# Performance work log

Hardware: AMD Instinct MI355X
Metric: run time of the kernel (lower is better)

## Reference

```python
import jax, jax.numpy as jnp
import numpy as np


def setup_inputs() -> dict:
    key = jax.random.key(0)
    ks = jax.random.split(key, 6)
    B, T, S, E, D = 8, 128, 512, 512, 512  # batch, trg_len, src_len, enc_dim, trg_dim
    W_SCALE = 0.03  # small init to keep tanh unsaturated
    return {
        "hidden": jax.random.normal(ks[0], (B, T, D), jnp.float32),
        "encoder_outputs": jax.random.normal(ks[1], (B, S, E), jnp.float32),
        "encoder_mask": jnp.ones((B, S), jnp.float32),
        "W_attn": jax.random.normal(ks[2], (D, E + D), jnp.float32) * W_SCALE,
        "b_attn": jnp.zeros((D,), jnp.float32),
        "W_v": jax.random.normal(ks[3], (1, D), jnp.float32) * W_SCALE,
        "b_v": jnp.zeros((1,), jnp.float32),
        "W_out": jax.random.normal(ks[4], (D, E + D), jnp.float32) * W_SCALE,
    }


def masked_softmax(x, m, axis=-1):
    # faithful to repo: x*m, stable exp, e*m, normalize with eps
    x = x * m
    e_x = jnp.exp(x - jnp.max(x, axis=axis, keepdims=True))
    e_x = e_x * m
    return e_x / (jnp.sum(e_x, axis=axis, keepdims=True) + 1e-6)


def reference(hidden, encoder_outputs, encoder_mask, W_attn, b_attn, W_v, b_v, W_out):
    B, T, D = hidden.shape
    S = encoder_outputs.shape[1]
    # concat order in get_energy is (hidden_i, encoder_outputs), so split W_attn
    W_h = W_attn[:, :D]   # (D_out, trg_dim)
    W_e = W_attn[:, D:]   # (D_out, enc_dim)
    # Linear(concat) == h@W_h^T + e@W_e^T + b; vectorized over all (t, s) pairs
    hp = jnp.einsum('btd,kd->btk', hidden, W_h)            # (B,T,K)
    ep = jnp.einsum('bse,ke->bsk', encoder_outputs, W_e)   # (B,S,K)
    feat = jnp.tanh(hp[:, :, None, :] + ep[:, None, :, :] + b_attn)  # (B,T,S,K)
    energies = jnp.einsum('btsk,k->bts', feat, W_v[0]) + b_v[0]      # (B,T,S)
    # forward: energies * mask, then masked softmax
    m = encoder_mask[:, None, :]  # (B,1,S)
    energies = energies * m
    attn_weights = masked_softmax(energies, m, axis=-1)    # (B,T,S)
    weighted_context = jnp.einsum('bts,bse->bte', attn_weights, encoder_outputs)
    h_cat = jnp.concatenate([weighted_context, hidden], axis=-1)  # (B,T,E+D)
    h_tilde = jnp.tanh(jnp.einsum('btc,dc->btd', h_cat, W_out))   # (B,T,D)
    return h_tilde, weighted_context, attn_weights
```

## Files before the change

### kernel.cpp

```cpp
#include <hip/hip_runtime.h>
#include <hip/hip_bf16.h>
#include <math.h>

typedef unsigned short u16;
typedef unsigned int u32;
typedef __bf16 bf16x8 __attribute__((ext_vector_type(8)));
typedef float f32x4 __attribute__((ext_vector_type(4)));

#define OUT_WC   524288LL
#define OUT_ATTN 1048576LL
#define C2 2.8853900817779268f
#define LOG2E 1.4426950408889634f
#define LAS 40

#define P_ENC    0LL
#define P_HID    2097152LL
#define P_WATTN  2621440LL
#define P_WOUTR  3145728LL
#define P_WOUTTL 3407872LL

__device__ inline u16 f2b(float f) {
    return (u16)((__float_as_uint(f) + 0x8000u) >> 16);
}
__device__ inline float b2f(u16 v) { return __uint_as_float(((u32)v) << 16); }
__device__ inline u32 pkcvt(float x, float y) {
    __hip_bfloat162 h = __float22bfloat162_rn(make_float2(x, y));
    return *(u32*)&h;
}
__device__ inline float tanh_fast(float x) {
    return 1.f - 2.f * __builtin_amdgcn_rcpf(__builtin_amdgcn_exp2f(C2 * x) + 1.f);
}

__global__ __launch_bounds__(256) void tobf(
    const float* __restrict__ enc, const float* __restrict__ hidden,
    const float* __restrict__ Wattn, const float* __restrict__ Wout,
    u16* __restrict__ dst)
{
    const int tid = threadIdx.x;
    if (blockIdx.x < 1664) {
        long long i = ((long long)blockIdx.x * 256 + tid) * 8;
        const float* src;
        if (i < 2097152)      src = enc + i;
        else if (i < 2621440) src = hidden + (i - 2097152);
        else if (i < 3145728) src = Wattn + (i - 2621440);
        else {
            long long j = i - 3145728;
            src = Wout + ((j >> 9) << 10) + 512 + (j & 511);
        }
        float4 v0 = *(const float4*)src;
        float4 v1 = *(const float4*)(src + 4);
        *(uint4*)(dst + i) = make_uint4(pkcvt(v0.x, v0.y), pkcvt(v0.z, v0.w),
                                        pkcvt(v1.x, v1.y), pkcvt(v1.z, v1.w));
    } else {
        __shared__ u32 lt[64 * 66];
        int tt = blockIdx.x - 1664;
        int n0 = (tt >> 3) * 64, d0 = (tt & 7) * 64;
        int r = tid >> 2, c = (tid & 3) * 16;
        const float* sp = Wout + (long long)(n0 + r) * 1024 + d0 + c;
        #pragma unroll
        for (int q = 0; q < 4; ++q) {
            float4 v = *(const float4*)(sp + q * 4);
            lt[r * 66 + c + q * 4 + 0] = f2b(v.x);
            lt[r * 66 + c + q * 4 + 1] = f2b(v.y);
            lt[r * 66 + c + q * 4 + 2] = f2b(v.z);
            lt[r * 66 + c + q * 4 + 3] = f2b(v.w);
        }
        __syncthreads();
        int dr = tid >> 2, nc = (tid & 3) * 16;
        u32 o[8];
        #pragma unroll
        for (int q = 0; q < 8; ++q) {
            u32 lo = lt[(nc + 2 * q) * 66 + dr];
            u32 hi = lt[(nc + 2 * q + 1) * 66 + dr];
            o[q] = lo | (hi << 16);
        }
        u16* dp = dst + P_WOUTTL + (long long)(d0 + dr) * 512 + n0 + nc;
        *(uint4*)dp       = make_uint4(o[0], o[1], o[2], o[3]);
        *(uint4*)(dp + 8) = make_uint4(o[4], o[5], o[6], o[7]);
    }
}

__global__ __launch_bounds__(256) void proj(
    const u16* __restrict__ pool, const float* __restrict__ battn,
    float* __restrict__ hp, u16* __restrict__ ept, float* __restrict__ hh)
{
    __shared__ u16 lA[64 * LAS];
    __shared__ u16 lB[64 * LAS];
    const int tid = threadIdx.x;
    const int wvi = tid >> 6, ln = tid & 63;
    const int wm = wvi >> 1, wn = wvi & 1;
    const int l16 = ln & 15, quad = ln >> 4;
    const int blk = blockIdx.x;
    int bx, by, zz = 0, lda, ldb, mode;
    const u16 *A, *B;
    if (blk < 512) {
        mode = 0;
        zz = blk >> 6; by = (blk >> 3) & 7; bx = blk & 7;
        A = pool + P_WATTN + 512; lda = 1024;
        B = pool + P_ENC + (long long)zz * 262144; ldb = 512;
    } else if (blk < 640) {
        mode = 1;
        int i = blk - 512; by = i >> 3; bx = i & 7;
        A = pool + P_HID; lda = 512;
        B = pool + P_WATTN; ldb = 1024;
    } else {
        mode = 2;
        int i = blk - 640; by = i >> 3; bx = i & 7;
        A = pool + P_HID; lda = 512;
        B = pool + P_WOUTR; ldb = 512;
    }
    const int m0 = by * 64, n0 = bx * 64;
    const int srow = tid >> 2, skof = (tid & 3) * 8;
    const u16* Ap = A + (long long)(m0 + srow) * lda + skof;
    const u16* Bp = B + (long long)(n0 + srow) * ldb + skof;

    f32x4 acc00 = {0,0,0,0}, acc01 = {0,0,0,0}, acc10 = {0,0,0,0}, acc11 = {0,0,0,0};

    for (int k0 = 0; k0 < 512; k0 += 32) {
        uint4 av = *(const uint4*)(Ap + k0);
        uint4 bv = *(const uint4*)(Bp + k0);
        __syncthreads();
        *(uint4*)&lA[srow * LAS + skof] = av;
        *(uint4*)&lB[srow * LAS + skof] = bv;
        __syncthreads();
        bf16x8 a0 = *(const bf16x8*)&lA[(wm * 32      + l16) * LAS + quad * 8];
        bf16x8 a1 = *(const bf16x8*)&lA[(wm * 32 + 16 + l16) * LAS + quad * 8];
        bf16x8 b0 = *(const bf16x8*)&lB[(wn * 32      + l16) * LAS + quad * 8];
        bf16x8 b1 = *(const bf16x8*)&lB[(wn * 32 + 16 + l16) * LAS + quad * 8];
        acc00 = __builtin_amdgcn_mfma_f32_16x16x32_bf16(a0, b0, acc00, 0, 0, 0);
        acc01 = __builtin_amdgcn_mfma_f32_16x16x32_bf16(a0, b1, acc01, 0, 0, 0);
        acc10 = __builtin_amdgcn_mfma_f32_16x16x32_bf16(a1, b0, acc10, 0, 0, 0);
        acc11 = __builtin_amdgcn_mfma_f32_16x16x32_bf16(a1, b1, acc11, 0, 0, 0);
    }

    const f32x4* accs[4] = { &acc00, &acc01, &acc10, &acc11 };
    #pragma unroll
    for (int i = 0; i < 2; ++i) {
        #pragma unroll
        for (int j = 0; j < 2; ++j) {
            const f32x4& a = *accs[i * 2 + j];
            #pragma unroll
            for (int r = 0; r < 4; ++r) {
                int m = m0 + wm * 32 + i * 16 + quad * 4 + r;
                int n = n0 + wn * 32 + j * 16 + l16;
                float v = a[r];
                if (mode == 0)
                    ept[(long long)zz * 262144 + (long long)m * 512 + n] =
                        f2b(__builtin_amdgcn_exp2f(C2 * v));
                else if (mode == 1)
                    hp[(long long)m * 512 + n] = C2 * (v + battn[n]);
                else
                    hh[(long long)m * 512 + n] = v;
            }
        }
    }
}

__device__ inline float wred_sum(float v) {
    #pragma unroll
    for (int i = 32; i > 0; i >>= 1) v += __shfl_xor(v, i);
    return v;
}
__device__ inline float bred_sum8(float v, float* red, int tid) {
    v = wred_sum(v);
    __syncthreads();
    if ((tid & 63) == 0) red[tid >> 6] = v;
    __syncthreads();
    float s = 0.f;
    #pragma unroll
    for (int i = 0; i < 8; ++i) s += red[i];
    return s;
}
__device__ inline void bred2_max(float v0, float v1, float* red, int tid,
                                 float* o0, float* o1) {
    #pragma unroll
    for (int i = 32; i > 0; i >>= 1) {
        v0 = fmaxf(v0, __shfl_xor(v0, i));
        v1 = fmaxf(v1, __shfl_xor(v1, i));
    }
    __syncthreads();
    if ((tid & 63) == 0) { red[tid >> 6] = v0; red[8 + (tid >> 6)] = v1; }
    __syncthreads();
    float a0 = red[0], a1 = red[8];
    #pragma unroll
    for (int i = 1; i < 8; ++i) { a0 = fmaxf(a0, red[i]); a1 = fmaxf(a1, red[8 + i]); }
    *o0 = a0; *o1 = a1;
}
__device__ inline void bred2_sum(float v0, float v1, float* red, int tid,
                                 float* o0, float* o1) {
    #pragma unroll
    for (int i = 32; i > 0; i >>= 1) { v0 += __shfl_xor(v0, i); v1 += __shfl_xor(v1, i); }
    __syncthreads();
    if ((tid & 63) == 0) { red[tid >> 6] = v0; red[8 + (tid >> 6)] = v1; }
    __syncthreads();
    float a0 = 0.f, a1 = 0.f;
    #pragma unroll
    for (int i = 0; i < 8; ++i) { a0 += red[i]; a1 += red[8 + i]; }
    *o0 = a0; *o1 = a1;
}

__device__ inline void proc8(uint4 c, float4 hw, float* a0, float* a1) {
    u32 cc[4] = {c.x, c.y, c.z, c.w};
    #pragma unroll
    for (int i = 0; i < 4; ++i) {
        float xl = __uint_as_float(cc[i] << 16);
        float xh = __uint_as_float(cc[i] & 0xFFFF0000u);
        float rl0 = __builtin_amdgcn_rcpf(fmaf(hw.x, xl, 1.f));
        float rh0 = __builtin_amdgcn_rcpf(fmaf(hw.x, xh, 1.f));
        float rl1 = __builtin_amdgcn_rcpf(fmaf(hw.y, xl, 1.f));
        float rh1 = __builtin_amdgcn_rcpf(fmaf(hw.y, xh, 1.f));
        a0[2*i]   = fmaf(hw.z, rl0, a0[2*i]);
        a0[2*i+1] = fmaf(hw.z, rh0, a0[2*i+1]);
        a1[2*i]   = fmaf(hw.z, rl1, a1[2*i]);
        a1[2*i+1] = fmaf(hw.z, rh1, a1[2*i+1]);
    }
}

__global__ __launch_bounds__(512) void energies(
    const float* __restrict__ maskp, const float* __restrict__ hp,
    const u16* __restrict__ ept, const float* __restrict__ Wv,
    const float* __restrict__ bvp, const u16* __restrict__ pool,
    float* __restrict__ out)
{
    __shared__ __align__(16) float4 hpw[512];
    __shared__ float pa[2][8][512];
    __shared__ __align__(16) float2 aL[512];
    __shared__ __align__(16) float2 wcL[512];
    __shared__ float red[16];
    const int tid = threadIdx.x;
    const int b = blockIdx.x >> 6;
    const int t0 = (blockIdx.x & 63) * 2;
    const u16* enc_bf = pool + P_ENC;
    const u16* woutT  = pool + P_WOUTTL;

    float w = Wv[tid];
    float h0 = hp[(long long)(b * 128 + t0) * 512 + tid];
    float h1 = hp[(long long)(b * 128 + t0 + 1) * 512 + tid];
    hpw[tid] = make_float4(__builtin_amdgcn_exp2f(h0), __builtin_amdgcn_exp2f(h1), w, 0.f);
    float sumWv = bred_sum8(w, red, tid);

    const int kg = tid >> 6, sl = tid & 63;
    const int s0 = sl * 8;
    const u16* eb = ept + (long long)b * 262144 + (kg * 64) * 512 + s0;
    const float4* hq = &hpw[kg * 64];

    float a0[8] = {0,0,0,0,0,0,0,0}, a1[8] = {0,0,0,0,0,0,0,0};
    uint4 c0 = *(const uint4*)(eb);
    uint4 c1 = *(const uint4*)(eb + 512);
    uint4 c2 = *(const uint4*)(eb + 1024);
    uint4 c3 = *(const uint4*)(eb + 1536);
    for (int kk = 0; kk < 60; kk += 4) {
        const u16* nb = eb + (kk + 4) * 512;
        uint4 n0 = *(const uint4*)(nb);
        uint4 n1 = *(const uint4*)(nb + 512);
        uint4 n2 = *(const uint4*)(nb + 1024);
        uint4 n3 = *(const uint4*)(nb + 1536);
        proc8(c0, hq[kk],     a0, a1);
        proc8(c1, hq[kk + 1], a0, a1);
        proc8(c2, hq[kk + 2], a0, a1);
        proc8(c3, hq[kk + 3], a0, a1);
        c0 = n0; c1 = n1; c2 = n2; c3 = n3;
    }
    proc8(c0, hq[60], a0, a1);
    proc8(c1, hq[61], a0, a1);
    proc8(c2, hq[62], a0, a1);
    proc8(c3, hq[63], a0, a1);

    *(float4*)&pa[0][kg][s0]     = make_float4(a0[0], a0[1], a0[2], a0[3]);
    *(float4*)&pa[0][kg][s0 + 4] = make_float4(a0[4], a0[5], a0[6], a0[7]);
    *(float4*)&pa[1][kg][s0]     = make_float4(a1[0], a1[1], a1[2], a1[3]);
    *(float4*)&pa[1][kg][s0 + 4] = make_float4(a1[4], a1[5], a1[6], a1[7]);
    __syncthreads();

    const int s = tid;
    float A0 = 0.f, A1 = 0.f;
    #pragma unroll
    for (int g = 0; g < 8; ++g) { A0 += pa[0][g][s]; A1 += pa[1][g][s]; }
    float mv = maskp[(long long)b * 512 + s];
    float bv0 = bvp[0];
    float r0 = (bv0 + sumWv - 2.f * A0) * mv; r0 *= mv;
    float r1 = (bv0 + sumWv - 2.f * A1) * mv; r1 *= mv;

    float mx0, mx1;
    bred2_max(r0, r1, red, tid, &mx0, &mx1);
    float ex0 = __builtin_amdgcn_exp2f((r0 - mx0) * LOG2E) * mv;
    float ex1 = __builtin_amdgcn_exp2f((r1 - mx1) * LOG2E) * mv;
    float sm0, sm1;
    bred2_sum(ex0, ex1, red, tid, &sm0, &sm1);
    float at0 = ex0 * (1.f / (sm0 + 1e-6f));
    float at1 = ex1 * (1.f / (sm1 + 1e-6f));
    out[OUT_ATTN + (long long)(b * 128 + t0) * 512 + s]     = at0;
    out[OUT_ATTN + (long long)(b * 128 + t0 + 1) * 512 + s] = at1;
    aL[s] = make_float2(at0, at1);
    __syncthreads();

    {
        const u16* encb = enc_bf + (long long)b * 262144 + tid;
        const float4* aL4 = (const float4*)aL;
        float acc0 = 0.f, acc1 = 0.f;
        for (int ss = 0; ss < 512; ss += 8) {
            float ev[8];
            #pragma unroll
            for (int i = 0; i < 8; ++i) ev[i] = b2f(encb[(ss + i) * 512]);
            #pragma unroll
            for (int i = 0; i < 4; ++i) {
                float4 ap = aL4[(ss >> 1) + i];
                acc0 = fmaf(ap.x, ev[2*i],   acc0);
                acc1 = fmaf(ap.y, ev[2*i],   acc1);
                acc0 = fmaf(ap.z, ev[2*i+1], acc0);
                acc1 = fmaf(ap.w, ev[2*i+1], acc1);
            }
        }
        out[OUT_WC + (long long)(b * 128 + t0) * 512 + tid]     = acc0;
        out[OUT_WC + (long long)(b * 128 + t0 + 1) * 512 + tid] = acc1;
        wcL[tid] = make_float2(acc0, acc1);
    }
    __syncthreads();

    {
        const u16* wt = woutT + tid;
        const float4* wL4 = (const float4*)wcL;
        float acc0 = 0.f, acc1 = 0.f;
        for (int dd = 0; dd < 512; dd += 8) {
            float wv[8];
            #pragma unroll
            for (int i = 0; i < 8; ++i) wv[i] = b2f(wt[(dd + i) * 512]);
            #pragma unroll
            for (int i = 0; i < 4; ++i) {
                float4 cp = wL4[(dd >> 1) + i];
                acc0 = fmaf(cp.x, wv[2*i],   acc0);
                acc1 = fmaf(cp.y, wv[2*i],   acc1);
                acc0 = fmaf(cp.z, wv[2*i+1], acc0);
                acc1 = fmaf(cp.w, wv[2*i+1], acc1);
            }
        }
        long long o0 = (long long)(b * 128 + t0) * 512 + tid;
        long long o1 = (long long)(b * 128 + t0 + 1) * 512 + tid;
        out[o0] = tanh_fast(acc0 + out[o0]);
        out[o1] = tanh_fast(acc1 + out[o1]);
    }
}

extern "C" void kernel_launch(void* const* d_in, const int* in_sizes, int n_in,
                              void* d_out, int out_size, void* d_ws, size_t ws_size,
                              hipStream_t stream)
{
    const float* hidden = (const float*)d_in[0];
    const float* enc    = (const float*)d_in[1];
    const float* mask   = (const float*)d_in[2];
    const float* Wattn  = (const float*)d_in[3];
    const float* battn  = (const float*)d_in[4];
    const float* Wv     = (const float*)d_in[5];
    const float* bvp    = (const float*)d_in[6];
    const float* Wout   = (const float*)d_in[7];
    float* out = (float*)d_out;

    float* hp  = (float*)d_ws;
    u16*   ept = (u16*)((char*)d_ws + (2 << 20));
    u16*   pool = (u16*)((char*)d_ws + (6 << 20));

    tobf<<<1728, 256, 0, stream>>>(enc, hidden, Wattn, Wout, pool);
    proj<<<768, 256, 0, stream>>>(pool, battn, hp, ept, out );
    energies<<<512, 512, 0, stream>>>(mask, hp, ept, Wv, bvp, pool, out);
}
```

Before: 153.5 us.

## Double energies block threads with split-K reductions and prefetch proj GEMM tiles

```diff
diff --git a/kernel.cpp b/kernel.cpp
--- a/kernel.cpp
+++ b/kernel.cpp
@@ -11,7 +11,7 @@
 #define OUT_ATTN 1048576LL
 #define C2 2.8853900817779268f
 #define LOG2E 1.4426950408889634f
-#define LAS 40
+#define PLAS 72
 
 #define P_ENC    0LL
 #define P_HID    2097152LL
@@ -84,8 +84,8 @@
     const u16* __restrict__ pool, const float* __restrict__ battn,
     float* __restrict__ hp, u16* __restrict__ ept, float* __restrict__ hh)
 {
-    __shared__ u16 lA[64 * LAS];
-    __shared__ u16 lB[64 * LAS];
+    __shared__ u16 lA[64 * PLAS];
+    __shared__ u16 lB[64 * PLAS];
     const int tid = threadIdx.x;
     const int wvi = tid >> 6, ln = tid & 63;
     const int wm = wvi >> 1, wn = wvi & 1;
@@ -110,40 +110,51 @@
         B = pool + P_WOUTR; ldb = 512;
     }
     const int m0 = by * 64, n0 = bx * 64;
-    const int srow = tid >> 2, skof = (tid & 3) * 8;
-    const u16* Ap = A + (long long)(m0 + srow) * lda + skof;
-    const u16* Bp = B + (long long)(n0 + srow) * ldb + skof;
-
-    f32x4 acc00 = {0,0,0,0}, acc01 = {0,0,0,0}, acc10 = {0,0,0,0}, acc11 = {0,0,0,0};
-
-    for (int k0 = 0; k0 < 512; k0 += 32) {
-        uint4 av = *(const uint4*)(Ap + k0);
-        uint4 bv = *(const uint4*)(Bp + k0);
-        __syncthreads();
-        *(uint4*)&lA[srow * LAS + skof] = av;
-        *(uint4*)&lB[srow * LAS + skof] = bv;
-        __syncthreads();
-        bf16x8 a0 = *(const bf16x8*)&lA[(wm * 32      + l16) * LAS + quad * 8];
-        bf16x8 a1 = *(const bf16x8*)&lA[(wm * 32 + 16 + l16) * LAS + quad * 8];
-        bf16x8 b0 = *(const bf16x8*)&lB[(wn * 32      + l16) * LAS + quad * 8];
-        bf16x8 b1 = *(const bf16x8*)&lB[(wn * 32 + 16 + l16) * LAS + quad * 8];
-        acc00 = __builtin_amdgcn_mfma_f32_16x16x32_bf16(a0, b0, acc00, 0, 0, 0);
-        acc01 = __builtin_amdgcn_mfma_f32_16x16x32_bf16(a0, b1, acc01, 0, 0, 0);
-        acc10 = __builtin_amdgcn_mfma_f32_16x16x32_bf16(a1, b0, acc10, 0, 0, 0);
-        acc11 = __builtin_amdgcn_mfma_f32_16x16x32_bf16(a1, b1, acc11, 0, 0, 0);
-    }
-
-    const f32x4* accs[4] = { &acc00, &acc01, &acc10, &acc11 };
+    const int sr = tid >> 2, sc = (tid & 3) * 16;
+    const u16* Ap = A + (long long)(m0 + sr) * lda + sc;
+    const u16* Bp = B + (long long)(n0 + sr) * ldb + sc;
+
+    f32x4 acc[2][2] = {};
+    uint4 ra0 = *(const uint4*)(Ap);
+    uint4 ra1 = *(const uint4*)(Ap + 8);
+    uint4 rb0 = *(const uint4*)(Bp);
+    uint4 rb1 = *(const uint4*)(Bp + 8);
+
+    for (int k0 = 0; k0 < 512; k0 += 64) {
+        __syncthreads();
+        *(uint4*)&lA[sr * PLAS + sc]     = ra0;
+        *(uint4*)&lA[sr * PLAS + sc + 8] = ra1;
+        *(uint4*)&lB[sr * PLAS + sc]     = rb0;
+        *(uint4*)&lB[sr * PLAS + sc + 8] = rb1;
+        __syncthreads();
+        if (k0 < 448) {
+            ra0 = *(const uint4*)(Ap + k0 + 64);
+            ra1 = *(const uint4*)(Ap + k0 + 72);
+            rb0 = *(const uint4*)(Bp + k0 + 64);
+            rb1 = *(const uint4*)(Bp + k0 + 72);
+        }
+        #pragma unroll
+        for (int kk = 0; kk < 2; ++kk) {
+            bf16x8 a0 = *(const bf16x8*)&lA[(wm * 32      + l16) * PLAS + kk * 32 + quad * 8];
+            bf16x8 a1 = *(const bf16x8*)&lA[(wm * 32 + 16 + l16) * PLAS + kk * 32 + quad * 8];
+            bf16x8 b0 = *(const bf16x8*)&lB[(wn * 32      + l16) * PLAS + kk * 32 + quad * 8];
+            bf16x8 b1 = *(const bf16x8*)&lB[(wn * 32 + 16 + l16) * PLAS + kk * 32 + quad * 8];
+            acc[0][0] = __builtin_amdgcn_mfma_f32_16x16x32_bf16(a0, b0, acc[0][0], 0, 0, 0);
+            acc[0][1] = __builtin_amdgcn_mfma_f32_16x16x32_bf16(a0, b1, acc[0][1], 0, 0, 0);
+            acc[1][0] = __builtin_amdgcn_mfma_f32_16x16x32_bf16(a1, b0, acc[1][0], 0, 0, 0);
+            acc[1][1] = __builtin_amdgcn_mfma_f32_16x16x32_bf16(a1, b1, acc[1][1], 0, 0, 0);
+        }
+    }
+
     #pragma unroll
     for (int i = 0; i < 2; ++i) {
         #pragma unroll
         for (int j = 0; j < 2; ++j) {
-            const f32x4& a = *accs[i * 2 + j];
             #pragma unroll
             for (int r = 0; r < 4; ++r) {
                 int m = m0 + wm * 32 + i * 16 + quad * 4 + r;
                 int n = n0 + wn * 32 + j * 16 + l16;
-                float v = a[r];
+                float v = acc[i][j][r];
                 if (mode == 0)
                     ept[(long long)zz * 262144 + (long long)m * 512 + n] =
                         f2b(__builtin_amdgcn_exp2f(C2 * v));
@@ -161,42 +172,42 @@
     for (int i = 32; i > 0; i >>= 1) v += __shfl_xor(v, i);
     return v;
 }
-__device__ inline float bred_sum8(float v, float* red, int tid) {
+__device__ inline float wred_max(float v) {
+    #pragma unroll
+    for (int i = 32; i > 0; i >>= 1) v = fmaxf(v, __shfl_xor(v, i));
+    return v;
+}
+__device__ inline float bred_sum16(float v, float* red, int tid) {
     v = wred_sum(v);
     __syncthreads();
     if ((tid & 63) == 0) red[tid >> 6] = v;
     __syncthreads();
     float s = 0.f;
     #pragma unroll
-    for (int i = 0; i < 8; ++i) s += red[i];
+    for (int i = 0; i < 16; ++i) s += red[i];
     return s;
 }
-__device__ inline void bred2_max(float v0, float v1, float* red, int tid,
-                                 float* o0, float* o1) {
-    #pragma unroll
-    for (int i = 32; i > 0; i >>= 1) {
-        v0 = fmaxf(v0, __shfl_xor(v0, i));
-        v1 = fmaxf(v1, __shfl_xor(v1, i));
-    }
-    __syncthreads();
-    if ((tid & 63) == 0) { red[tid >> 6] = v0; red[8 + (tid >> 6)] = v1; }
-    __syncthreads();
-    float a0 = red[0], a1 = red[8];
-    #pragma unroll
-    for (int i = 1; i < 8; ++i) { a0 = fmaxf(a0, red[i]); a1 = fmaxf(a1, red[8 + i]); }
-    *o0 = a0; *o1 = a1;
-}
-__device__ inline void bred2_sum(float v0, float v1, float* red, int tid,
-                                 float* o0, float* o1) {
-    #pragma unroll
-    for (int i = 32; i > 0; i >>= 1) { v0 += __shfl_xor(v0, i); v1 += __shfl_xor(v1, i); }
-    __syncthreads();
-    if ((tid & 63) == 0) { red[tid >> 6] = v0; red[8 + (tid >> 6)] = v1; }
-    __syncthreads();
-    float a0 = 0.f, a1 = 0.f;
-    #pragma unroll
-    for (int i = 0; i < 8; ++i) { a0 += red[i]; a1 += red[8 + i]; }
-    *o0 = a0; *o1 = a1;
+__device__ inline float bred_rowmax(float v, float* red, int tid) {
+    v = wred_max(v);
+    __syncthreads();
+    if ((tid & 63) == 0) red[tid >> 6] = v;
+    __syncthreads();
+    int base = (tid >> 9) * 8;
+    float m = red[base];
+    #pragma unroll
+    for (int i = 1; i < 8; ++i) m = fmaxf(m, red[base + i]);
+    return m;
+}
+__device__ inline float bred_rowsum(float v, float* red, int tid) {
+    v = wred_sum(v);
+    __syncthreads();
+    if ((tid & 63) == 0) red[tid >> 6] = v;
+    __syncthreads();
+    int base = (tid >> 9) * 8;
+    float s = 0.f;
+    #pragma unroll
+    for (int i = 0; i < 8; ++i) s += red[base + i];
+    return s;
 }
 
 __device__ inline void proc8(uint4 c, float4 hw, float* a0, float* a1) {
@@ -216,40 +227,43 @@
     }
 }
 
-__global__ __launch_bounds__(512) void energies(
+__global__ __launch_bounds__(1024, 8) void energies(
     const float* __restrict__ maskp, const float* __restrict__ hp,
     const u16* __restrict__ ept, const float* __restrict__ Wv,
     const float* __restrict__ bvp, const u16* __restrict__ pool,
     float* __restrict__ out)
 {
     __shared__ __align__(16) float4 hpw[512];
-    __shared__ float pa[2][8][512];
-    __shared__ __align__(16) float2 aL[512];
-    __shared__ __align__(16) float2 wcL[512];
+    __shared__ float pa[2][16][512];
     __shared__ float red[16];
+    float* aLf = (float*)hpw;
+    float2* wcL = ((float2*)hpw) + 512;
     const int tid = threadIdx.x;
     const int b = blockIdx.x >> 6;
     const int t0 = (blockIdx.x & 63) * 2;
     const u16* enc_bf = pool + P_ENC;
     const u16* woutT  = pool + P_WOUTTL;
 
-    float w = Wv[tid];
-    float h0 = hp[(long long)(b * 128 + t0) * 512 + tid];
-    float h1 = hp[(long long)(b * 128 + t0 + 1) * 512 + tid];
-    hpw[tid] = make_float4(__builtin_amdgcn_exp2f(h0), __builtin_amdgcn_exp2f(h1), w, 0.f);
-    float sumWv = bred_sum8(w, red, tid);
+    float w = 0.f;
+    if (tid < 512) {
+        w = Wv[tid];
+        float h0 = hp[(long long)(b * 128 + t0) * 512 + tid];
+        float h1 = hp[(long long)(b * 128 + t0 + 1) * 512 + tid];
+        hpw[tid] = make_float4(__builtin_amdgcn_exp2f(h0), __builtin_amdgcn_exp2f(h1), w, 0.f);
+    }
+    float sumWv = bred_sum16(w, red, tid);
 
     const int kg = tid >> 6, sl = tid & 63;
     const int s0 = sl * 8;
-    const u16* eb = ept + (long long)b * 262144 + (kg * 64) * 512 + s0;
-    const float4* hq = &hpw[kg * 64];
+    const u16* eb = ept + (long long)b * 262144 + (kg * 32) * 512 + s0;
+    const float4* hq = &hpw[kg * 32];
 
     float a0[8] = {0,0,0,0,0,0,0,0}, a1[8] = {0,0,0,0,0,0,0,0};
     uint4 c0 = *(const uint4*)(eb);
     uint4 c1 = *(const uint4*)(eb + 512);
     uint4 c2 = *(const uint4*)(eb + 1024);
     uint4 c3 = *(const uint4*)(eb + 1536);
-    for (int kk = 0; kk < 60; kk += 4) {
+    for (int kk = 0; kk < 28; kk += 4) {
         const u16* nb = eb + (kk + 4) * 512;
         uint4 n0 = *(const uint4*)(nb);
         uint4 n1 = *(const uint4*)(nb + 512);
@@ -261,10 +275,10 @@
         proc8(c3, hq[kk + 3], a0, a1);
         c0 = n0; c1 = n1; c2 = n2; c3 = n3;
     }
-    proc8(c0, hq[60], a0, a1);
-    proc8(c1, hq[61], a0, a1);
-    proc8(c2, hq[62], a0, a1);
-    proc8(c3, hq[63], a0, a1);
+    proc8(c0, hq[28], a0, a1);
+    proc8(c1, hq[29], a0, a1);
+    proc8(c2, hq[30], a0, a1);
+    proc8(c3, hq[31], a0, a1);
 
     *(float4*)&pa[0][kg][s0]     = make_float4(a0[0], a0[1], a0[2], a0[3]);
     *(float4*)&pa[0][kg][s0 + 4] = make_float4(a0[4], a0[5], a0[6], a0[7]);
@@ -272,36 +286,35 @@
     *(float4*)&pa[1][kg][s0 + 4] = make_float4(a1[4], a1[5], a1[6], a1[7]);
     __syncthreads();
 
-    const int s = tid;
-    float A0 = 0.f, A1 = 0.f;
-    #pragma unroll
-    for (int g = 0; g < 8; ++g) { A0 += pa[0][g][s]; A1 += pa[1][g][s]; }
+    const int rr = tid >> 9, s = tid & 511;
+    float A = 0.f;
+    #pragma unroll
+    for (int g = 0; g < 16; ++g) A += pa[rr][g][s];
     float mv = maskp[(long long)b * 512 + s];
-    float bv0 = bvp[0];
-    float r0 = (bv0 + sumWv - 2.f * A0) * mv; r0 *= mv;
-    float r1 = (bv0 + sumWv - 2.f * A1) * mv; r1 *= mv;
-
-    float mx0, mx1;
-    bred2_max(r0, r1, red, tid, &mx0, &mx1);
-    float ex0 = __builtin_amdgcn_exp2f((r0 - mx0) * LOG2E) * mv;
-    float ex1 = __builtin_amdgcn_exp2f((r1 - mx1) * LOG2E) * mv;
-    float sm0, sm1;
-    bred2_sum(ex0, ex1, red, tid, &sm0, &sm1);
-    float at0 = ex0 * (1.f / (sm0 + 1e-6f));
-    float at1 = ex1 * (1.f / (sm1 + 1e-6f));
-    out[OUT_ATTN + (long long)(b * 128 + t0) * 512 + s]     = at0;
-    out[OUT_ATTN + (long long)(b * 128 + t0 + 1) * 512 + s] = at1;
-    aL[s] = make_float2(at0, at1);
-    __syncthreads();
+    float r = (bvp[0] + sumWv - 2.f * A) * mv; r *= mv;
+    float mx = bred_rowmax(r, red, tid);
+    float ex = __builtin_amdgcn_exp2f((r - mx) * LOG2E) * mv;
+    float sm = bred_rowsum(ex, red, tid);
+    float at = ex * (1.f / (sm + 1e-6f));
+    out[OUT_ATTN + (long long)(b * 128 + t0 + rr) * 512 + s] = at;
+    aLf[s * 2 + rr] = at;
+    __syncthreads();
+
+    const float* wp = (const float*)pa;
+    float* wpw = (float*)pa;
+    const int half = tid >> 9, e = tid & 511;
 
     {
-        const u16* encb = enc_bf + (long long)b * 262144 + tid;
-        const float4* aL4 = (const float4*)aL;
+        const u16* encb = enc_bf + (long long)b * 262144 + (long long)(half * 256) * 512 + e;
+        const float4* aL4 = (const float4*)aLf + half * 128;
         float acc0 = 0.f, acc1 = 0.f;
-        for (int ss = 0; ss < 512; ss += 8) {
-            float ev[8];
-            #pragma unroll
-            for (int i = 0; i < 8; ++i) ev[i] = b2f(encb[(ss + i) * 512]);
+        float ev[8];
+        #pragma unroll
+        for (int i = 0; i < 8; ++i) ev[i] = b2f(encb[i * 512]);
+        for (int ss = 0; ss < 248; ss += 8) {
+            float nv[8];
+            #pragma unroll
+            for (int i = 0; i < 8; ++i) nv[i] = b2f(encb[(ss + 8 + i) * 512]);
             #pragma unroll
             for (int i = 0; i < 4; ++i) {
                 float4 ap = aL4[(ss >> 1) + i];
@@ -310,21 +323,40 @@
                 acc0 = fmaf(ap.z, ev[2*i+1], acc0);
                 acc1 = fmaf(ap.w, ev[2*i+1], acc1);
             }
-        }
-        out[OUT_WC + (long long)(b * 128 + t0) * 512 + tid]     = acc0;
-        out[OUT_WC + (long long)(b * 128 + t0 + 1) * 512 + tid] = acc1;
-        wcL[tid] = make_float2(acc0, acc1);
-    }
-    __syncthreads();
+            #pragma unroll
+            for (int i = 0; i < 8; ++i) ev[i] = nv[i];
+        }
+        #pragma unroll
+        for (int i = 0; i < 4; ++i) {
+            float4 ap = aL4[124 + i];
+            acc0 = fmaf(ap.x, ev[2*i],   acc0);
+            acc1 = fmaf(ap.y, ev[2*i],   acc1);
+            acc0 = fmaf(ap.z, ev[2*i+1], acc0);
+            acc1 = fmaf(ap.w, ev[2*i+1], acc1);
+        }
+        if (half) { wpw[e] = acc0; wpw[512 + e] = acc1; }
+        __syncthreads();
+        if (!half) {
+            acc0 += wp[e]; acc1 += wp[512 + e];
+            out[OUT_WC + (long long)(b * 128 + t0) * 512 + e]     = acc0;
+            out[OUT_WC + (long long)(b * 128 + t0 + 1) * 512 + e] = acc1;
+            wcL[e] = make_float2(acc0, acc1);
+        }
+        __syncthreads();
+    }
 
     {
-        const u16* wt = woutT + tid;
-        const float4* wL4 = (const float4*)wcL;
+        const int n = e;
+        const u16* wt = woutT + (long long)(half * 256) * 512 + n;
+        const float4* wL4 = (const float4*)wcL + half * 128;
         float acc0 = 0.f, acc1 = 0.f;
-        for (int dd = 0; dd < 512; dd += 8) {
-            float wv[8];
-            #pragma unroll
-            for (int i = 0; i < 8; ++i) wv[i] = b2f(wt[(dd + i) * 512]);
+        float wv[8];
+        #pragma unroll
+        for (int i = 0; i < 8; ++i) wv[i] = b2f(wt[i * 512]);
+        for (int dd = 0; dd < 248; dd += 8) {
+            float nv[8];
+            #pragma unroll
+            for (int i = 0; i < 8; ++i) nv[i] = b2f(wt[(dd + 8 + i) * 512]);
             #pragma unroll
             for (int i = 0; i < 4; ++i) {
                 float4 cp = wL4[(dd >> 1) + i];
@@ -333,11 +365,27 @@
                 acc0 = fmaf(cp.z, wv[2*i+1], acc0);
                 acc1 = fmaf(cp.w, wv[2*i+1], acc1);
             }
-        }
-        long long o0 = (long long)(b * 128 + t0) * 512 + tid;
-        long long o1 = (long long)(b * 128 + t0 + 1) * 512 + tid;
-        out[o0] = tanh_fast(acc0 + out[o0]);
-        out[o1] = tanh_fast(acc1 + out[o1]);
+            #pragma unroll
+            for (int i = 0; i < 8; ++i) wv[i] = nv[i];
+        }
+        #pragma unroll
+        for (int i = 0; i < 4; ++i) {
+            float4 cp = wL4[124 + i];
+            acc0 = fmaf(cp.x, wv[2*i],   acc0);
+            acc1 = fmaf(cp.y, wv[2*i],   acc1);
+            acc0 = fmaf(cp.z, wv[2*i+1], acc0);
+            acc1 = fmaf(cp.w, wv[2*i+1], acc1);
+        }
+        __syncthreads();
+        if (half) { wpw[n] = acc0; wpw[512 + n] = acc1; }
+        __syncthreads();
+        if (!half) {
+            acc0 += wp[n]; acc1 += wp[512 + n];
+            long long o0 = (long long)(b * 128 + t0) * 512 + n;
+            long long o1 = (long long)(b * 128 + t0 + 1) * 512 + n;
+            out[o0] = tanh_fast(acc0 + out[o0]);
+            out[o1] = tanh_fast(acc1 + out[o1]);
+        }
     }
 }
 
@@ -361,5 +409,5 @@
 
     tobf<<<1728, 256, 0, stream>>>(enc, hidden, Wattn, Wout, pool);
     proj<<<768, 256, 0, stream>>>(pool, battn, hp, ept, out );
-    energies<<<512, 512, 0, stream>>>(mask, hp, ept, Wv, bvp, pool, out);
-}
+    energies<<<512, 1024, 0, stream>>>(mask, hp, ept, Wv, bvp, pool, out);
+}
```

New measurement: 194.5 us. +26.7%, slower.
